# Optimization experiments

Hardware: AMD Instinct MI355X
Metric: run time of the kernel (lower is better)

## Reference

```python
import jax, jax.numpy as jnp
import numpy as np

G = 64        # grid_size
S = 4         # num_samples along perpendicular axis
C = 771       # feature_channels
NH = 3        # n_heads
NV = 4        # number of camera views
HF = WF = 64  # image feature map size
B = 1
QD = 3 * C    # query_dim of TriplaneAttention


def bilin(img, gx, gy, padding):
    """Bilinear grid_sample, align_corners=True. img [C,H,W]; gx,gy normalized [-1,1]."""
    Ci, H, W = img.shape
    ix = (gx + 1.0) * 0.5 * (W - 1)
    iy = (gy + 1.0) * 0.5 * (H - 1)
    if padding == 'border':
        ix = jnp.clip(ix, 0, W - 1)
        iy = jnp.clip(iy, 0, H - 1)
    x0 = jnp.floor(ix); y0 = jnp.floor(iy)
    x1 = x0 + 1.0;      y1 = y0 + 1.0
    wx = ix - x0;       wy = iy - y0
    img2 = img.reshape(Ci, H * W)
    def gather(xi, yi):
        xc = jnp.clip(xi, 0, W - 1).astype(jnp.int32)
        yc = jnp.clip(yi, 0, H - 1).astype(jnp.int32)
        vals = jnp.take(img2, (yc * W + xc).reshape(-1), axis=1).reshape((Ci,) + xi.shape)
        if padding == 'zeros':
            valid = ((xi >= 0) & (xi <= W - 1) & (yi >= 0) & (yi <= H - 1)).astype(img.dtype)
            vals = vals * valid
        return vals
    return (gather(x0, y0) * ((1 - wx) * (1 - wy)) + gather(x1, y0) * (wx * (1 - wy))
            + gather(x0, y1) * ((1 - wx) * wy) + gather(x1, y1) * (wx * wy))


def sample_points_along_axis(plane):
    x = jnp.linspace(-1.0, 1.0, G)
    gx, gy = jnp.meshgrid(x, x, indexing='xy')  # [G,G]
    samp = jnp.linspace(-1.0, 1.0, S)
    ex = jnp.broadcast_to(gx[..., None], (G, G, S))
    ey = jnp.broadcast_to(gy[..., None], (G, G, S))
    es = jnp.broadcast_to(samp[None, None, :], (G, G, S))
    if plane == 'xy':
        return jnp.stack([ex, ey, es], axis=-1)
    elif plane == 'xz':
        return jnp.stack([ex, es, ey], axis=-1)
    else:
        return jnp.stack([es, ex, ey], axis=-1)


def project_to_other_planes(points, plane, queries):
    # points [G,G,S,3]; queries = [q_xy, q_xz, q_yz] each [G,G,C]
    idx = {'xy': 0, 'xz': 1, 'yz': 2}
    sel = {'xy': (0, 1), 'xz': (0, 2), 'yz': (1, 2)}
    feats = []
    for other in ['xy', 'xz', 'yz']:
        if other == plane:
            continue
        a, b = sel[other]
        coords = jnp.stack([points[..., a], points[..., b]], axis=-1)
        # Faithful to original: pixel-range coords passed as normalized grid, border padding
        g = jnp.clip((coords * 0.5 + 0.5) * (G - 1), 0, G - 1)
        pf = queries[idx[other]].transpose(2, 0, 1)  # [C,G,G]
        s = bilin(pf, g[..., 0], g[..., 1], 'border')  # [C,G,G,S]
        feats.append(s.transpose(1, 2, 3, 0))          # [G,G,S,C]
    return jnp.concatenate(feats, axis=2)              # [G,G,2S,C]


def layernorm(x, g, b):
    mu = jnp.mean(x, axis=-1, keepdims=True)
    var = jnp.mean((x - mu) ** 2, axis=-1, keepdims=True)
    return (x - mu) / jnp.sqrt(var + 1e-5) * g + b


def triplane_attention(query, context, Wk, bk, Wv, bv, ln_g, ln_b):
    # query [B,N,QD]; context [B,N,L,C]
    Bq, N, L, _ = context.shape
    DH = QD // NH
    q = layernorm(query, ln_g, ln_b).reshape(Bq, N, NH, DH)
    k = (context @ Wk + bk).reshape(Bq, N, L, NH, DH)
    v = (context @ Wv + bv).reshape(Bq, N, L, NH, DH)
    scores = jnp.einsum('bnlhd,bnhd->bhnl', k, q)   # no 1/sqrt(d) scaling (faithful)
    w = jax.nn.softmax(scores, axis=-1)
    out = jnp.einsum('bhnl,bnlhd->bnhd', w, v)
    return out.reshape(Bq, N, QD)


def setup_inputs():
    key = jax.random.key(0)
    ks = jax.random.split(key, 12)
    image_features = jax.random.normal(ks[0], (B, NV, C, HF, WF), jnp.float32)
    depths = jax.random.uniform(ks[1], (B, NV, HF, WF), jnp.float32)
    # cameras: identity rotation, w2c translation [dx,0,3] -> c2w translation [-dx,0,-3]
    offs = np.linspace(-0.2, 0.2, NV).astype(np.float32)
    c2w = np.tile(np.eye(4, dtype=np.float32), (B, NV, 1, 1))
    for m in range(NV):
        c2w[:, m, 0, 3] = -offs[m]
        c2w[:, m, 2, 3] = -3.0
    K = np.zeros((B, NV, 3, 3), np.float32)
    K[:, :, 0, 0] = WF; K[:, :, 1, 1] = HF
    K[:, :, 0, 2] = WF / 2; K[:, :, 1, 2] = HF / 2; K[:, :, 2, 2] = 1.0
    pointclouds = jax.random.uniform(ks[2], (B, 4096, 3), jnp.float32, minval=-1.0, maxval=1.0)
    q_xy = jax.random.normal(ks[3], (G, G, C), jnp.float32) * 0.02
    q_xz = jax.random.normal(ks[4], (G, G, C), jnp.float32) * 0.02
    q_yz = jax.random.normal(ks[5], (G, G, C), jnp.float32) * 0.02
    Wk = jax.random.normal(ks[6], (C, QD), jnp.float32) * 0.02
    bk = jnp.zeros((QD,), jnp.float32)
    Wv = jax.random.normal(ks[7], (C, QD), jnp.float32) * 0.02
    bv = jnp.zeros((QD,), jnp.float32)
    ln_g = jnp.ones((QD,), jnp.float32)
    ln_b = jnp.zeros((QD,), jnp.float32)
    return dict(image_features=image_features, depths=depths, c2w_cond=jnp.asarray(c2w),
                intrinsic_cond=jnp.asarray(K), pointclouds=pointclouds,
                q_xy=q_xy, q_xz=q_xz, q_yz=q_yz, Wk=Wk, bk=bk, Wv=Wv, bv=bv,
                ln_g=ln_g, ln_b=ln_b)


def _forward(image_features, c2w_cond, intrinsic_cond, q_xy, q_xz, q_yz,
             Wk, bk, Wv, bv, ln_g, ln_b):
    queries = [q_xy, q_xz, q_yz]
    w2c = jnp.linalg.inv(c2w_cond)  # [B,NV,4,4]

    def project(pts, w2c_b, K_b):
        # pts [N,3]; returns u,v,mask each [N,NV]
        ph = jnp.concatenate([pts, jnp.ones_like(pts[:, :1])], axis=-1)
        cam = jnp.einsum('nl,mkl->nmk', ph, w2c_b)      # [N,NV,4]
        depth = cam[..., 2]
        uvh = jnp.einsum('nmk,mhk->nmh', cam[..., :3], K_b)
        ds = depth + 1e-8
        u = uvh[..., 0] / ds
        v = uvh[..., 1] / ds
        mask = (depth > 0) & (u >= 0) & (u < WF) & (v >= 0) & (v < HF)
        return u, v, mask

    def sample_views(feats_b, u_b, v_b, mask_b):
        # feats_b [NV,C,HF,WF]; u_b,v_b [N,NV] -> [N,NV,C]
        gx = 2.0 * (u_b / (WF - 1)) - 1.0
        gy = 2.0 * (v_b / (HF - 1)) - 1.0
        samp = jax.vmap(lambda img, x, y: bilin(img, x, y, 'zeros'))(feats_b, gx.T, gy.T)  # [NV,C,N]
        samp = samp.transpose(2, 0, 1)  # [N,NV,C]
        return samp * mask_b[..., None].astype(samp.dtype)

    outs = []
    for pi, plane in enumerate(['xy', 'xz', 'yz']):
        points = sample_points_along_axis(plane)           # [G,G,S,3]
        pts = points.reshape(-1, 3)                        # [G*G*S,3]
        u, v, mask = jax.vmap(lambda w, k: project(pts, w, k))(w2c, intrinsic_cond)  # [B,N,NV]
        samp = jax.vmap(sample_views)(image_features, u, v, mask)  # [B,N,NV,C]
        ctx = samp.reshape(B, G * G, S * NV, C)
        other = project_to_other_planes(points, plane, queries)    # [G,G,2S,C]
        q = jnp.concatenate([queries[pi],
                             jnp.mean(other[:, :, :S], axis=2),
                             jnp.mean(other[:, :, S:], axis=2)], axis=-1).reshape(G * G, QD)
        q = jnp.broadcast_to(q[None], (B, G * G, QD))
        out = triplane_attention(q, ctx, Wk, bk, Wv, bv, ln_g, ln_b)
        outs.append(out.reshape(B, G, G, QD))
    return tuple(outs)


def reference(image_features, depths, c2w_cond, intrinsic_cond, pointclouds,
              q_xy, q_xz, q_yz, Wk, bk, Wv, bv, ln_g, ln_b):
    return _forward(image_features, c2w_cond, intrinsic_cond,
                    q_xy, q_xz, q_yz, Wk, bk, Wv, bv, ln_g, ln_b)
```

## Files before the change

### kernel.cpp

```cpp
#include <hip/hip_runtime.h>
#include <math.h>


constexpr int kG = 64, kS = 4, kC = 771, kNV = 4;
constexpr int kQD = 2313;
constexpr int kNPIX = 4096;
constexpr int kL = 16;
constexpr int kImgMStride = kC * kG * kG;
constexpr int kKP = 800;
constexpr int kLDA = 2400;
constexpr int kBROWS = 896;
constexpr int kCP = 776;
constexpr int kNG = kCP / 4;
constexpr int kLDQ = 3 * kCP;
constexpr int kIMS2 = kNPIX * kCP;

constexpr size_t kQKB_FLOATS = (size_t)kNPIX * kLDQ;
constexpr size_t kW_ELEMS = (size_t)3 * kBROWS * kKP;
constexpr size_t kA0_ELEMS = (size_t)kNPIX * kKP;
constexpr size_t kWH_ELEMS = (size_t)kNPIX * kLDA;
constexpr size_t kQN_FLOATS = (size_t)kNPIX * kQD;
constexpr size_t kTAB_FLOATS = (size_t)6 * 64 * kC;

using bf16x8 = __attribute__((ext_vector_type(8))) short;
// ... 387 lines not shown
        for (int r = 0; r < 4; ++r) {
          const int row = rbase + i * 16 + (lane >> 4) * 4 + r;
          const float mu = mr[2 * row], rs = mr[2 * row + 1];
          dst[(size_t)row * kLDQ + col] = rs * acc[i][j][r] - rs * mu * uu + vv;
        }
      } else if (col < kCP) {
#pragma unroll
        for (int r = 0; r < 4; ++r) {
          const int row = rbase + i * 16 + (lane >> 4) * 4 + r;
          dst[(size_t)row * kLDQ + col] = 0.f;
        }
      }
    }
  }
}

__global__ void __launch_bounds__(256) gemm_tab_kernel(
    const unsigned short* __restrict__ Thi,
    const unsigned short* __restrict__ Tlo,
    const unsigned short* __restrict__ Wkhi,
    const unsigned short* __restrict__ Wklo, float* __restrict__ Atab) {
  __shared__ unsigned short smA[2][128 * 32];
  __shared__ unsigned short smB[2][128 * 32];
  const int t = blockIdx.y;
  const int n0 = blockIdx.x * 128;
  const int h = 1 + (t & 1);
  const unsigned short* Ah = Thi + (size_t)t * 128 * kKP;
  const unsigned short* Al = Tlo + (size_t)t * 128 * kKP;
  const unsigned short* Bh = Wkhi + (size_t)h * kBROWS * kKP;
  const unsigned short* Bl = Wklo + (size_t)h * kBROWS * kKP;
  const int tid = threadIdx.x;
  const int lane = tid & 63, w = tid >> 6;
  const int wm = w >> 1, wn = w & 1;

  const int sr0 = w * 16 + (lane >> 2);
  const int ss = lane & 3;
  size_t aoff[2], boff[2];
  int ldsb[2];
#pragma unroll
  for (int p = 0; p < 2; ++p) {
    const int r = p * 64 + sr0;
    const int kl = (ss ^ ((r >> 1) & 3)) * 8;
    aoff[p] = (size_t)r * kKP + kl;
    boff[p] = (size_t)(n0 + r) * kKP + kl;
    ldsb[p] = (p * 64 + w * 16) * 32;
  }
  int offA[4], offB[4];
#pragma unroll
  for (int i = 0; i < 4; ++i) {
    const int ra = wm * 64 + i * 16 + (lane & 15);
    offA[i] = ra * 32 + (((lane >> 4) ^ ((ra >> 1) & 3)) << 3);
    const int rb = wn * 64 + i * 16 + (lane & 15);
    offB[i] = rb * 32 + (((lane >> 4) ^ ((rb >> 1) & 3)) << 3);
  }
  f32x4 acc[4][4];
#pragma unroll
  for (int i = 0; i < 4; ++i)
#pragma unroll
    for (int j = 0; j < 4; ++j) acc[i][j] = f32x4{0.f, 0.f, 0.f, 0.f};

  for (int k0 = 0; k0 < kKP; k0 += 32) {
#pragma unroll
    for (int p = 0; p < 2; ++p) {
      gload16(Ah + aoff[p] + k0, &smA[0][ldsb[p]]);
      gload16(Al + aoff[p] + k0, &smA[1][ldsb[p]]);
      gload16(Bh + boff[p] + k0, &smB[0][ldsb[p]]);
      gload16(Bl + boff[p] + k0, &smB[1][ldsb[p]]);
    }
    __syncthreads();
    bf16x8 ah[4], al[4], bh[4], bl[4];
#pragma unroll
    for (int i = 0; i < 4; ++i) {
      ah[i] = *(const bf16x8*)&smA[0][offA[i]];
      al[i] = *(const bf16x8*)&smA[1][offA[i]];
      bh[i] = *(const bf16x8*)&smB[0][offB[i]];
      bl[i] = *(const bf16x8*)&smB[1][offB[i]];
    }
#pragma unroll
    for (int i = 0; i < 4; ++i)
#pragma unroll
      for (int j = 0; j < 4; ++j)
        acc[i][j] = __builtin_amdgcn_mfma_f32_16x16x32_bf16(ah[i], bh[j],
                                                            acc[i][j], 0, 0, 0);
#pragma unroll
    for (int i = 0; i < 4; ++i)
#pragma unroll
      for (int j = 0; j < 4; ++j)
        acc[i][j] = __builtin_amdgcn_mfma_f32_16x16x32_bf16(ah[i], bl[j],
                                                            acc[i][j], 0, 0, 0);
#pragma unroll
    for (int i = 0; i < 4; ++i)
#pragma unroll
      for (int j = 0; j < 4; ++j)
        acc[i][j] = __builtin_amdgcn_mfma_f32_16x16x32_bf16(al[i], bh[j],
                                                            acc[i][j], 0, 0, 0);
    __syncthreads();
  }

  float* C = Atab + (size_t)t * 128 * kCP;
  const int rbase = wm * 64;
  const int cbase = n0 + wn * 64;
#pragma unroll
  for (int i = 0; i < 4; ++i) {
#pragma unroll
    for (int j = 0; j < 4; ++j) {
      const int col = cbase + j * 16 + (lane & 15);
      if (col < kCP) {
        const float keep = (col < kC) ? 1.f : 0.f;
#pragma unroll
        for (int r = 0; r < 4; ++r) {
          const int row = rbase + i * 16 + (lane >> 4) * 4 + r;
          C[(size_t)row * kCP + col] = acc[i][j][r] * keep;
        }
      }
    }
  }
}

__global__ void __launch_bounds__(256) combine_qk_kernel(
    const float* __restrict__ Atab, const float* __restrict__ u,
    const float* __restrict__ v, const float* __restrict__ murs,
    float* __restrict__ qkb) {
  const int slot = blockIdx.y, n = blockIdx.x;
  const int i = n >> 6, j = n & 63, tid = threadIdx.x;
  const float mu = murs[2 * ((size_t)slot * kNPIX + n)];
  const float rs = murs[2 * ((size_t)slot * kNPIX + n) + 1];
  const float rsmu = rs * mu;
  float* dst = qkb + (size_t)slot * kQKB_FLOATS + (size_t)n * kLDQ;
  const float* A1 = Atab + ((size_t)(slot * 2 + 0) * 128 + j) * kCP;
  const float* A2 = Atab + ((size_t)(slot * 2 + 1) * 128 + i) * kCP;
  if (tid < kNG) {
    const int c4 = tid << 2;
    const float4 a1 = *(const float4*)&A1[c4];
    const float4 u1 = *(const float4*)&u[kCP + c4];
    const float4 v1 = *(const float4*)&v[kCP + c4];
    float4 r1;
    r1.x = rs * a1.x - rsmu * u1.x + v1.x;
    r1.y = rs * a1.y - rsmu * u1.y + v1.y;
    r1.z = rs * a1.z - rsmu * u1.z + v1.z;
    r1.w = rs * a1.w - rsmu * u1.w + v1.w;
    *(float4*)&dst[kCP + c4] = r1;
    const float4 a2 = *(const float4*)&A2[c4];
    const float4 u2 = *(const float4*)&u[2 * kCP + c4];
    const float4 v2 = *(const float4*)&v[2 * kCP + c4];
    float4 r2;
    r2.x = rs * a2.x - rsmu * u2.x + v2.x;
    r2.y = rs * a2.y - rsmu * u2.y + v2.y;
    r2.z = rs * a2.z - rsmu * u2.z + v2.z;
    r2.w = rs * a2.w - rsmu * u2.w + v2.w;
    *(float4*)&dst[2 * kCP + c4] = r2;
  }
}

__global__ void __launch_bounds__(512, 6) sample_attn4_kernel(
    const float* __restrict__ imgt, const float* __restrict__ w2c,
    const float* __restrict__ Kin, const float* __restrict__ qkb,
    const float* __restrict__ qbk, unsigned short* __restrict__ whi) {
  __shared__ __align__(16) float ctx[kL][kCP];
  __shared__ float sW2[kL][4];
  __shared__ int sI2[kL][4];
  __shared__ float sscp[2][48];
  __shared__ float ssc[48], swt[48];
  const int slot = blockIdx.y, plane = slot;
  const int bid = blockIdx.x;
  const int xcd = bid & 7, tt = bid >> 3;
  const int i = (xcd << 3) | ((tt >> 3) & 7);
  const int j = (((tt >> 6) << 3) | (tt & 7));
  const int n = (i << 6) | j;
  const int tid = threadIdx.x;
  const float* qkn = qkb + (size_t)slot * kQKB_FLOATS + (size_t)n * kLDQ;

  if (tid < kL) {
    const int s = tid >> 2, m = tid & 3;
    const float Xi = -1.f + 2.f * i / 63.f;
    const float Xj = -1.f + 2.f * j / 63.f;
    const float Ts = -1.f + 2.f * s / 3.f;
    float px, py, pz;
    if (plane == 0) { px = Xj; py = Xi; pz = Ts; }
    else if (plane == 1) { px = Xj; py = Ts; pz = Xi; }
    else { px = Ts; py = Xj; pz = Xi; }
    const float* W = w2c + m * 16;
    const float c0 = W[0] * px + W[1] * py + W[2] * pz + W[3];
    const float c1 = W[4] * px + W[5] * py + W[6] * pz + W[7];
    const float c2 = W[8] * px + W[9] * py + W[10] * pz + W[11];
    const float* Km = Kin + m * 9;
    const float un = Km[0] * c0 + Km[1] * c1 + Km[2] * c2;
    const float vn = Km[3] * c0 + Km[4] * c1 + Km[5] * c2;
    const float ds = c2 + 1e-8f;
    const float u = un / ds, v = vn / ds;
    const bool mk =
        (c2 > 0.f && u >= 0.f && u < 64.f && v >= 0.f && v < 64.f);
    float w00 = 0.f, w10 = 0.f, w01 = 0.f, w11 = 0.f;
    int i00 = 0, i10 = 0, i01 = 0, i11 = 0;
    if (mk) {
      const float gx = 2.f * (u / 63.f) - 1.f;
      const float gy = 2.f * (v / 63.f) - 1.f;
      const float ix = (gx + 1.f) * 0.5f * 63.f;
      const float iy = (gy + 1.f) * 0.5f * 63.f;
      const float x0 = floorf(ix), y0 = floorf(iy);
      const float x1 = x0 + 1.f, y1 = y0 + 1.f;
      const float wx = ix - x0, wy = iy - y0;
      const float v00 = (x0 >= 0.f && x0 <= 63.f && y0 >= 0.f && y0 <= 63.f) ? 1.f : 0.f;
      const float v10 = (x1 >= 0.f && x1 <= 63.f && y0 >= 0.f && y0 <= 63.f) ? 1.f : 0.f;
      const float v01 = (x0 >= 0.f && x0 <= 63.f && y1 >= 0.f && y1 <= 63.f) ? 1.f : 0.f;
      const float v11 = (x1 >= 0.f && x1 <= 63.f && y1 >= 0.f && y1 <= 63.f) ? 1.f : 0.f;
      w00 = (1.f - wx) * (1.f - wy) * v00;
      w10 = wx * (1.f - wy) * v10;
      w01 = (1.f - wx) * wy * v01;
      w11 = wx * wy * v11;
      const int x0i = (int)fminf(fmaxf(x0, 0.f), 63.f);
      const int x1i = (int)fminf(fmaxf(x1, 0.f), 63.f);
      const int y0i = (int)fminf(fmaxf(y0, 0.f), 63.f);
      const int y1i = (int)fminf(fmaxf(y1, 0.f), 63.f);
      const int mb = m * kIMS2;
      i00 = mb + (y0i * 64 + x0i) * kCP;
      i10 = mb + (y0i * 64 + x1i) * kCP;
      i01 = mb + (y1i * 64 + x0i) * kCP;
      i11 = mb + (y1i * 64 + x1i) * kCP;
    }
    sI2[tid][0] = i00; sI2[tid][1] = i10; sI2[tid][2] = i01; sI2[tid][3] = i11;
    sW2[tid][0] = w00; sW2[tid][1] = w10; sW2[tid][2] = w01; sW2[tid][3] = w11;
  }
  __syncthreads();

  const int lane = tid & 63, wv = tid >> 6;
#pragma unroll
  for (int q = 0; q < 2; ++q) {
    const int l = (wv << 1) + q;
    const float a0 = sW2[l][0], a1 = sW2[l][1], a2 = sW2[l][2], a3 = sW2[l][3];
    const int b0 = sI2[l][0], b1 = sI2[l][1], b2 = sI2[l][2], b3 = sI2[l][3];
    for (int g = lane; g < kNG; g += 64) {
      const int c4 = g << 2;
      const float4 t0 = *(const float4*)&imgt[b0 + c4];
      const float4 t1 = *(const float4*)&imgt[b1 + c4];
      const float4 t2 = *(const float4*)&imgt[b2 + c4];
      const float4 t3 = *(const float4*)&imgt[b3 + c4];
      float4 r;
      r.x = fmaf(t0.x, a0, fmaf(t1.x, a1, fmaf(t2.x, a2, t3.x * a3)));
      r.y = fmaf(t0.y, a0, fmaf(t1.y, a1, fmaf(t2.y, a2, t3.y * a3)));
      r.z = fmaf(t0.z, a0, fmaf(t1.z, a1, fmaf(t2.z, a2, t3.z * a3)));
      r.w = fmaf(t0.w, a0, fmaf(t1.w, a1, fmaf(t2.w, a2, t3.w * a3)));
      *(float4*)&ctx[l][c4] = r;
    }
  }
  __syncthreads();

  const int g16 = tid >> 4, l16 = tid & 15;
  const float* qbkn = qbk + ((size_t)slot * kNPIX + n) * 3;
  {
    const int l = g16 & 15, half = g16 >> 4;
    float p0 = 0.f, p1 = 0.f, p2 = 0.f;
#pragma unroll
    for (int it = 0; it < 6; ++it) {
      const int c4 = (l16 + ((2 * it + half) << 4)) << 2;
      const float4 cv = *(const float4*)&ctx[l][c4];
      const float4 q0 = *(const float4*)&qkn[c4];
      const float4 q1 = *(const float4*)&qkn[kCP + c4];
      const float4 q2 = *(const float4*)&qkn[2 * kCP + c4];
      p0 = fmaf(cv.x, q0.x, fmaf(cv.y, q0.y, fmaf(cv.z, q0.z, fmaf(cv.w, q0.w, p0))));
      p1 = fmaf(cv.x, q1.x, fmaf(cv.y, q1.y, fmaf(cv.z, q1.z, fmaf(cv.w, q1.w, p1))));
      p2 = fmaf(cv.x, q2.x, fmaf(cv.y, q2.y, fmaf(cv.z, q2.z, fmaf(cv.w, q2.w, p2))));
    }
    if (half == 0 && l16 < 2) {
      const int c4 = (192 + l16) << 2;
      const float4 cv = *(const float4*)&ctx[l][c4];
      const float4 q0 = *(const float4*)&qkn[c4];
      const float4 q1 = *(const float4*)&qkn[kCP + c4];
      const float4 q2 = *(const float4*)&qkn[2 * kCP + c4];
      p0 = fmaf(cv.x, q0.x, fmaf(cv.y, q0.y, fmaf(cv.z, q0.z, fmaf(cv.w, q0.w, p0))));
      p1 = fmaf(cv.x, q1.x, fmaf(cv.y, q1.y, fmaf(cv.z, q1.z, fmaf(cv.w, q1.w, p1))));
      p2 = fmaf(cv.x, q2.x, fmaf(cv.y, q2.y, fmaf(cv.z, q2.z, fmaf(cv.w, q2.w, p2))));
    }
#pragma unroll
    for (int off = 8; off; off >>= 1) {
      p0 += __shfl_down(p0, off, 16);
      p1 += __shfl_down(p1, off, 16);
      p2 += __shfl_down(p2, off, 16);
    }
    if (l16 == 0) {
      sscp[half][l] = p0;
      sscp[half][16 + l] = p1;
      sscp[half][32 + l] = p2;
    }
  }
  __syncthreads();
  if (tid < 48) ssc[tid] = sscp[0][tid] + sscp[1][tid] + qbkn[tid >> 4];
  __syncthreads();
  if (tid < 3) {
    float mx = ssc[tid * 16];
#pragma unroll
    for (int l = 1; l < kL; ++l) mx = fmaxf(mx, ssc[tid * 16 + l]);
    float e[kL];
    float sum = 0.f;
#pragma unroll
    for (int l = 0; l < kL; ++l) {
      e[l] = expf(ssc[tid * 16 + l] - mx);
      sum += e[l];
    }
    const float inv = 1.f / sum;
#pragma unroll
    for (int l = 0; l < kL; ++l) swt[tid * 16 + l] = e[l] * inv;
  }
  __syncthreads();

  unsigned short* wh = whi + (size_t)slot * kWH_ELEMS + (size_t)n * kLDA;
  if (tid < 2 * kNG) {
    const int c4 = (tid >> 1) << 2;
    const int l0 = (tid & 1) << 3;
    float4 o0{0.f, 0.f, 0.f, 0.f}, o1{0.f, 0.f, 0.f, 0.f},
        o2{0.f, 0.f, 0.f, 0.f};
#pragma unroll
    for (int dl = 0; dl < 8; ++dl) {
      const int l = l0 + dl;
      const float4 cv = *(const float4*)&ctx[l][c4];
      const float s0 = swt[l], s1 = swt[16 + l], s2 = swt[32 + l];
      o0.x = fmaf(cv.x, s0, o0.x); o0.y = fmaf(cv.y, s0, o0.y);
      o0.z = fmaf(cv.z, s0, o0.z); o0.w = fmaf(cv.w, s0, o0.w);
      o1.x = fmaf(cv.x, s1, o1.x); o1.y = fmaf(cv.y, s1, o1.y);
      o1.z = fmaf(cv.z, s1, o1.z); o1.w = fmaf(cv.w, s1, o1.w);
      o2.x = fmaf(cv.x, s2, o2.x); o2.y = fmaf(cv.y, s2, o2.y);
      o2.z = fmaf(cv.z, s2, o2.z); o2.w = fmaf(cv.w, s2, o2.w);
    }
    o0.x += __shfl_xor(o0.x, 1); o0.y += __shfl_xor(o0.y, 1);
    o0.z += __shfl_xor(o0.z, 1); o0.w += __shfl_xor(o0.w, 1);
    o1.x += __shfl_xor(o1.x, 1); o1.y += __shfl_xor(o1.y, 1);
    o1.z += __shfl_xor(o1.z, 1); o1.w += __shfl_xor(o1.w, 1);
    o2.x += __shfl_xor(o2.x, 1); o2.y += __shfl_xor(o2.y, 1);
    o2.z += __shfl_xor(o2.z, 1); o2.w += __shfl_xor(o2.w, 1);
    if ((tid & 1) == 0) {
      float4 ov[3] = {o0, o1, o2};
#pragma unroll
      for (int h = 0; h < 3; ++h) {
        ushort4 hi;
        hi.x = f2bf(ov[h].x);
        hi.y = f2bf(ov[h].y);
        hi.z = f2bf(ov[h].z);
        hi.w = f2bf(ov[h].w);
        *(ushort4*)&wh[h * kKP + c4] = hi;
      }
    }
  }
  if (tid < 72) {
    const int h = tid / 24, k2 = kCP + tid % 24;
    wh[h * kKP + k2] = 0;
  }
}

__global__ void __launch_bounds__(256) gemm_out_kernel(
    const unsigned short* __restrict__ Ahi,
    const unsigned short* __restrict__ Bhi, float* __restrict__ C,
    const float* __restrict__ bias) {
  __shared__ unsigned short smA[128 * 32];
  __shared__ unsigned short smB[128 * 32];
  const int slot = blockIdx.z / 3, h = blockIdx.z % 3;
  const int t = blockIdx.y * 7 + blockIdx.x;
  const int xcd = t & 7, idx = t >> 3;
  const int nb = idx % 7, mb = (xcd << 2) + idx / 7;
  const int m0 = mb * 128, n0 = nb * 128;
  const unsigned short* Ah = Ahi + (size_t)slot * kWH_ELEMS;
  float* Cs = C + (size_t)slot * kQN_FLOATS;
  const int tid = threadIdx.x;
  const int lane = tid & 63, w = tid >> 6;
  const int wm = w >> 1, wn = w & 1;

  const int sr0 = w * 16 + (lane >> 2);
  const int ss = lane & 3;
  size_t aoff[2], boff[2];
  int ldsb[2];
#pragma unroll
  for (int p = 0; p < 2; ++p) {
    const int r = p * 64 + sr0;
    const int kl = (ss ^ ((r >> 1) & 3)) * 8;
    aoff[p] = (size_t)(m0 + r) * kLDA + (size_t)h * kKP + kl;
    boff[p] = ((size_t)h * kBROWS + (n0 + r)) * kKP + kl;
    ldsb[p] = (p * 64 + w * 16) * 32;
  }
  int offA[4], offB[4];
#pragma unroll
  for (int i = 0; i < 4; ++i) {
    const int ra = wm * 64 + i * 16 + (lane & 15);
    offA[i] = ra * 32 + (((lane >> 4) ^ ((ra >> 1) & 3)) << 3);
    const int rb = wn * 64 + i * 16 + (lane & 15);
    offB[i] = rb * 32 + (((lane >> 4) ^ ((rb >> 1) & 3)) << 3);
  }
  f32x4 acc[4][4];
#pragma unroll
  for (int i = 0; i < 4; ++i)
#pragma unroll
    for (int j = 0; j < 4; ++j) acc[i][j] = f32x4{0.f, 0.f, 0.f, 0.f};

  for (int k0 = 0; k0 < kKP; k0 += 32) {
#pragma unroll
    for (int p = 0; p < 2; ++p) {
      gload16(Ah + aoff[p] + k0, &smA[ldsb[p]]);
      gload16(Bhi + boff[p] + k0, &smB[ldsb[p]]);
    }
    __syncthreads();
    bf16x8 ah[4], bh[4];
#pragma unroll
    for (int i = 0; i < 4; ++i) {
      ah[i] = *(const bf16x8*)&smA[offA[i]];
      bh[i] = *(const bf16x8*)&smB[offB[i]];
    }
#pragma unroll
    for (int i = 0; i < 4; ++i)
#pragma unroll
      for (int j = 0; j < 4; ++j)
        acc[i][j] = __builtin_amdgcn_mfma_f32_16x16x32_bf16(ah[i], bh[j],
                                                            acc[i][j], 0, 0, 0);
    __syncthreads();
  }

  const int rbase = m0 + wm * 64;
  const int cbase = n0 + wn * 64;
#pragma unroll
  for (int i = 0; i < 4; ++i) {
#pragma unroll
    for (int j = 0; j < 4; ++j) {
      const int col = cbase + j * 16 + (lane & 15);
      if (col < kC) {
        const float bb = bias[h * kC + col];
#pragma unroll
        for (int r = 0; r < 4; ++r) {
          const int row = rbase + i * 16 + (lane >> 4) * 4 + r;
          Cs[(size_t)row * kQD + h * kC + col] = acc[i][j][r] + bb;
        }
      }
    }
  }
}

__global__ void __launch_bounds__(256) build_q_f32(
    const float* __restrict__ q_xy, const float* __restrict__ q_xz,
    const float* __restrict__ q_yz, const int plane,
    const float* __restrict__ ln_g, const float* __restrict__ ln_b,
    const float* __restrict__ bk, float* __restrict__ qn,
    float* __restrict__ qbk) {
  const float* qp = (plane == 0) ? q_xy : (plane == 1) ? q_xz : q_yz;
  const float* qo0 = (plane == 0) ? q_xz : q_xy;
  const float* qo1 = (plane == 2) ? q_xz : q_yz;
  const int n = blockIdx.x, i = n >> 6, j = n & 63, tid = threadIdx.x;
  __shared__ float qf[kQD];
  __shared__ int sIdx[2][4][4];
  __shared__ float sW[2][4][4];
  __shared__ float red[16];

  if (tid < 8) {
    const int part = tid >> 2, s = tid & 3;
    const float Xi = -1.f + 2.f * i / 63.f;
    const float Xj = -1.f + 2.f * j / 63.f;
    const float Ts = -1.f + 2.f * s / 3.f;
    float a, b;
    if (plane == 0) { a = part ? Xi : Xj; b = Ts; }
    else if (plane == 1) {
      if (part == 0) { a = Xj; b = Ts; } else { a = Ts; b = Xi; }
    } else { a = Ts; b = part ? Xi : Xj; }
    const float ga = fminf(fmaxf((a * 0.5f + 0.5f) * 63.f, 0.f), 63.f);
    const float gb = fminf(fmaxf((b * 0.5f + 0.5f) * 63.f, 0.f), 63.f);
    const float ix = fminf(fmaxf((ga + 1.f) * 0.5f * 63.f, 0.f), 63.f);
    const float iy = fminf(fmaxf((gb + 1.f) * 0.5f * 63.f, 0.f), 63.f);
    const float x0 = floorf(ix), y0 = floorf(iy);
    const float wx = ix - x0, wy = iy - y0;
    const int x0i = (int)x0, y0i = (int)y0;
    const int x1i = (x0i + 1 > 63) ? 63 : x0i + 1;
    const int y1i = (y0i + 1 > 63) ? 63 : y0i + 1;
    sIdx[part][s][0] = (y0i * 64 + x0i) * kC;
    sIdx[part][s][1] = (y0i * 64 + x1i) * kC;
    sIdx[part][s][2] = (y1i * 64 + x0i) * kC;
    sIdx[part][s][3] = (y1i * 64 + x1i) * kC;
    sW[part][s][0] = (1.f - wx) * (1.f - wy);
    sW[part][s][1] = wx * (1.f - wy);
    sW[part][s][2] = (1.f - wx) * wy;
    sW[part][s][3] = wx * wy;
  }
  __syncthreads();
  for (int c = tid; c < kC; c += 256) {
    qf[c] = qp[(size_t)n * kC + c];
    float a1 = 0.f, a2 = 0.f;
#pragma unroll
    for (int s = 0; s < 4; ++s) {
      a1 += qo0[sIdx[0][s][0] + c] * sW[0][s][0]
          + qo0[sIdx[0][s][1] + c] * sW[0][s][1]
          + qo0[sIdx[0][s][2] + c] * sW[0][s][2]
          + qo0[sIdx[0][s][3] + c] * sW[0][s][3];
      a2 += qo1[sIdx[1][s][0] + c] * sW[1][s][0]
          + qo1[sIdx[1][s][1] + c] * sW[1][s][1]
          + qo1[sIdx[1][s][2] + c] * sW[1][s][2]
          + qo1[sIdx[1][s][3] + c] * sW[1][s][3];
    }
    qf[kC + c] = a1 * 0.25f;
    qf[2 * kC + c] = a2 * 0.25f;
// ... 191 lines not shown
  __shared__ float Bs[BK][BN + 4];
  const int hoff = blockIdx.z * hstride;
  const int m0 = blockIdx.y * BM, n0 = blockIdx.x * BN;
  const int tid = threadIdx.x;
  const int ty = tid >> 4, tx = tid & 15;
  float acc[8][4];
#pragma unroll
  for (int r = 0; r < 8; ++r)
#pragma unroll
    for (int c = 0; c < 4; ++c) acc[r][c] = 0.f;
  for (int k0 = 0; k0 < K; k0 += BK) {
#pragma unroll
    for (int p = 0; p < 8; ++p) {
      const int idx = tid + p * 256;
      const int mm = idx >> 4, kk = idx & 15;
      float v = 0.f;
      if (k0 + kk < K) v = A[(size_t)(m0 + mm) * lda + hoff + k0 + kk];
      As[kk][mm] = v;
    }
    if (BT) {
#pragma unroll
      for (int p = 0; p < 4; ++p) {
        const int idx = tid + p * 256;
        const int jj = idx >> 4, kk = idx & 15;
        float v = 0.f;
        if ((n0 + jj) < N && (k0 + kk) < K)
          v = B[(size_t)(n0 + jj) * ldb + hoff + k0 + kk];
        Bs[kk][jj] = v;
      }
    } else {
#pragma unroll
      for (int p = 0; p < 4; ++p) {
        const int idx = tid + p * 256;
        const int kk = idx >> 6, jj = idx & 63;
        float v = 0.f;
        if ((n0 + jj) < N && (k0 + kk) < K)
          v = B[(size_t)(k0 + kk) * ldb + hoff + n0 + jj];
        Bs[kk][jj] = v;
      }
    }
    __syncthreads();
#pragma unroll
    for (int kk = 0; kk < BK; ++kk) {
      float a[8], b[4];
#pragma unroll
      for (int r = 0; r < 8; ++r) a[r] = As[kk][ty * 8 + r];
#pragma unroll
      for (int c = 0; c < 4; ++c) b[c] = Bs[kk][tx * 4 + c];
#pragma unroll
      for (int r = 0; r < 8; ++r)
#pragma unroll
        for (int c = 0; c < 4; ++c) acc[r][c] = fmaf(a[r], b[c], acc[r][c]);
    }
    __syncthreads();
  }
#pragma unroll
  for (int r = 0; r < 8; ++r) {
    const int mm = m0 + ty * 8 + r;
    if (mm >= M) continue;
#pragma unroll
    for (int c = 0; c < 4; ++c) {
      const int jj = n0 + tx * 4 + c;
      if (jj < N) {
        float v = acc[r][c];
        if (BIAS) v += bias[hoff + jj];
        Cp[(size_t)mm * ldc + hoff + jj] = v;
      }
    }
  }
}

extern "C" void kernel_launch(void* const* d_in, const int* in_sizes, int n_in,
                              void* d_out, int out_size, void* d_ws,
                              size_t ws_size, hipStream_t stream) {
  const float* imgf = (const float*)d_in[0];
  const float* c2w = (const float*)d_in[2];
  const float* Kin = (const float*)d_in[3];
  const float* qpl[3] = {(const float*)d_in[5], (const float*)d_in[6],
                         (const float*)d_in[7]};
  const float* Wk = (const float*)d_in[8];
  const float* bk = (const float*)d_in[9];
  const float* Wv = (const float*)d_in[10];
  const float* bv = (const float*)d_in[11];
  const float* ln_g = (const float*)d_in[12];
  const float* ln_b = (const float*)d_in[13];
  float* out = (float*)d_out;
  char* wsb = (char*)d_ws;

  const size_t IMGT_FLOATS = (size_t)kNV * kIMS2;

  size_t off = 0;
  auto take = [&](size_t bytes) {
    size_t p = off;
    off = (off + bytes + 511) & ~(size_t)511;
    return p;
  };
  const size_t o_w2c = take(64 * 4);
  const size_t o_qbk = take((size_t)3 * kNPIX * 3 * 4);
  const size_t o_qkb = take((size_t)3 * kQKB_FLOATS * 4);
  const size_t o_wkhi = take(kW_ELEMS * 2);
  const size_t o_wklo = take(kW_ELEMS * 2);
  const size_t o_wvthi = take(kW_ELEMS * 2);
  const size_t o_a0hi = take((size_t)3 * kA0_ELEMS * 2);
  const size_t o_a0lo = take((size_t)3 * kA0_ELEMS * 2);
  const size_t o_whi = take((size_t)3 * kWH_ELEMS * 2);
  const size_t o_murs = take((size_t)3 * kNPIX * 2 * 4);
  const size_t o_u = take((size_t)3 * kCP * 4);
  const size_t o_v = take((size_t)3 * kCP * 4);
  const size_t o_tab = take(kTAB_FLOATS * 4);
  const size_t o_tshi = take((size_t)6 * 128 * kKP * 2);
  const size_t o_tslo = take((size_t)6 * 128 * kKP * 2);
  const size_t o_atab = take((size_t)6 * 128 * kCP * 4);
  const size_t o_imgt = take(IMGT_FLOATS * 4);
  const size_t need = off;

  if (ws_size >= need) {
    float* w2c = (float*)(wsb + o_w2c);
    float* qbk = (float*)(wsb + o_qbk);
    float* qkb = (float*)(wsb + o_qkb);
    unsigned short* wkhi = (unsigned short*)(wsb + o_wkhi);
    unsigned short* wklo = (unsigned short*)(wsb + o_wklo);
    unsigned short* wvthi = (unsigned short*)(wsb + o_wvthi);
    unsigned short* a0hi = (unsigned short*)(wsb + o_a0hi);
    unsigned short* a0lo = (unsigned short*)(wsb + o_a0lo);
    unsigned short* whi = (unsigned short*)(wsb + o_whi);
    float* murs = (float*)(wsb + o_murs);
    float* uvec = (float*)(wsb + o_u);
    float* vvec = (float*)(wsb + o_v);
    float* meantab = (float*)(wsb + o_tab);
    unsigned short* tshi = (unsigned short*)(wsb + o_tshi);
    unsigned short* tslo = (unsigned short*)(wsb + o_tslo);
    float* atab = (float*)(wsb + o_atab);
    float* imgt = (float*)(wsb + o_imgt);

    invert4_kernel<<<1, 64, 0, stream>>>(c2w, w2c);
    prep_wk_kernel<<<dim3(kBROWS, 3), 256, 0, stream>>>(Wk, wkhi, wklo);
    prep_wvt_kernel<<<dim3(13, 14, 3), 256, 0, stream>>>(Wv, wvthi);
    prep_meantab_kernel<<<dim3(64, 6), 256, 0, stream>>>(qpl[0], qpl[1],
                                                         qpl[2], meantab);
    prep_tabsplit_kernel<<<dim3(128, 6), 256, 0, stream>>>(meantab, ln_g,
                                                           tshi, tslo);
    prep_uv_kernel<<<dim3(kCP, 3), 256, 0, stream>>>(Wk, ln_g, ln_b, uvec,
                                                     vvec);
    transpose_img_kernel<<<dim3(64, kNV), 256, 0, stream>>>(imgf, imgt);
    gemm_tab_kernel<<<dim3(7, 6), 256, 0, stream>>>(tshi, tslo, wkhi, wklo,
                                                    atab);
    build_a0_kernel<<<dim3(kNPIX, 3), 256, 0, stream>>>(
        qpl[0], qpl[1], qpl[2], meantab, ln_g, ln_b, bk, a0hi, a0lo, murs,
        qbk);
    gemm_a0_kernel<<<dim3(7, 32, 3), 256, 0, stream>>>(
        a0hi, a0lo, wkhi, wklo, murs, uvec, vvec, qkb);
    combine_qk_kernel<<<dim3(kNPIX, 3), 256, 0, stream>>>(atab, uvec, vvec,
                                                          murs, qkb);
    sample_attn4_kernel<<<dim3(kNPIX, 3), 512, 0, stream>>>(
        imgt, w2c, Kin, qkb, qbk, whi);
    gemm_out_kernel<<<dim3(7, 32, 9), 256, 0, stream>>>(whi, wvthi, out, bv);
  } else {
    float* ws = (float*)d_ws;
    const size_t OFF_QBK = 64;
    const size_t OFF_BIG = OFF_QBK + (size_t)kNPIX * 3;
    float* w2c = ws;
    float* qbk = ws + OFF_QBK;
    float* qn = ws + OFF_BIG;
    float* qkb = qn + kQN_FLOATS;

    invert4_kernel<<<1, 64, 0, stream>>>(c2w, w2c);
    for (int p = 0; p < 3; ++p) {
      build_q_f32<<<kNPIX, 256, 0, stream>>>(qpl[0], qpl[1], qpl[2], p, ln_g,
                                             ln_b, bk, qn, qbk);
      gemm_f32<true, false><<<dim3(13, 32, 3), 256, 0, stream>>>(
          qn, Wk, qkb, nullptr, kNPIX, kC, kC, kQD, kQD, kQD, kC);
      sample_attn_f32<<<kNPIX, 256, 0, stream>>>(imgf, w2c, Kin, qkb, qbk, p,
                                                 qn);
      gemm_f32<false, true><<<dim3(13, 32, 3), 256, 0, stream>>>(
          qn, Wv, out + (size_t)p * kQN_FLOATS, bv, kNPIX, kC, kC, kQD, kQD,
          kQD, kC);
    }
  }
}
```

Measured before the change: 585.7 us.

## Process sampling-attention context in two chunks with online softmax to halve LDS

The fused sample+attention kernel now builds the 16-entry context in two chunks of 8 rows instead of holding all 16 rows in shared memory. Softmax becomes an online (running max/sum with rescale) update, and normalisation is deferred to the final write. This roughly halves shared memory per block, allowing launch bounds to rise from 6 to 8 blocks per CU for more latency hiding. In exchange it adds extra barriers, the rescale arithmetic, and more qk global loads (qkn is reread once per chunk).

```diff
diff --git a/kernel.cpp b/kernel.cpp
--- a/kernel.cpp
+++ b/kernel.cpp
@@ -563,15 +563,17 @@
   }
 }
 
-__global__ void __launch_bounds__(512, 6) sample_attn4_kernel(
+__global__ void __launch_bounds__(512, 8) sample_attn6_kernel(
     const float* __restrict__ imgt, const float* __restrict__ w2c,
     const float* __restrict__ Kin, const float* __restrict__ qkb,
     const float* __restrict__ qbk, unsigned short* __restrict__ whi) {
-  __shared__ __align__(16) float ctx[kL][kCP];
+  __shared__ __align__(16) float ctx8[8][kCP];
   __shared__ float sW2[kL][4];
   __shared__ int sI2[kL][4];
-  __shared__ float sscp[2][48];
-  __shared__ float ssc[48], swt[48];
+  __shared__ float sscp[4][24];
+  __shared__ float ssc[24];
+  __shared__ float swts[3][8];
+  __shared__ float smax[3], ssum[3], srf[3];
   const int slot = blockIdx.y, plane = slot;
   const int bid = blockIdx.x;
   const int xcd = bid & 7, tt = bid >> 3;
@@ -632,106 +634,128 @@
     sI2[tid][0] = i00; sI2[tid][1] = i10; sI2[tid][2] = i01; sI2[tid][3] = i11;
     sW2[tid][0] = w00; sW2[tid][1] = w10; sW2[tid][2] = w01; sW2[tid][3] = w11;
   }
+  if (tid < 3) {
+    smax[tid] = -INFINITY;
+    ssum[tid] = 0.f;
+  }
   __syncthreads();
 
   const int lane = tid & 63, wv = tid >> 6;
-#pragma unroll
-  for (int q = 0; q < 2; ++q) {
-    const int l = (wv << 1) + q;
-    const float a0 = sW2[l][0], a1 = sW2[l][1], a2 = sW2[l][2], a3 = sW2[l][3];
-    const int b0 = sI2[l][0], b1 = sI2[l][1], b2 = sI2[l][2], b3 = sI2[l][3];
-    for (int g = lane; g < kNG; g += 64) {
-      const int c4 = g << 2;
-      const float4 t0 = *(const float4*)&imgt[b0 + c4];
-      const float4 t1 = *(const float4*)&imgt[b1 + c4];
-      const float4 t2 = *(const float4*)&imgt[b2 + c4];
-      const float4 t3 = *(const float4*)&imgt[b3 + c4];
-      float4 r;
-      r.x = fmaf(t0.x, a0, fmaf(t1.x, a1, fmaf(t2.x, a2, t3.x * a3)));
-      r.y = fmaf(t0.y, a0, fmaf(t1.y, a1, fmaf(t2.y, a2, t3.y * a3)));
-      r.z = fmaf(t0.z, a0, fmaf(t1.z, a1, fmaf(t2.z, a2, t3.z * a3)));
-      r.w = fmaf(t0.w, a0, fmaf(t1.w, a1, fmaf(t2.w, a2, t3.w * a3)));
-      *(float4*)&ctx[l][c4] = r;
-    }
-  }
-  __syncthreads();
-
-  const int g16 = tid >> 4, l16 = tid & 15;
   const float* qbkn = qbk + ((size_t)slot * kNPIX + n) * 3;
-  {
-    const int l = g16 & 15, half = g16 >> 4;
-    float p0 = 0.f, p1 = 0.f, p2 = 0.f;
-#pragma unroll
-    for (int it = 0; it < 6; ++it) {
-      const int c4 = (l16 + ((2 * it + half) << 4)) << 2;
-      const float4 cv = *(const float4*)&ctx[l][c4];
-      const float4 q0 = *(const float4*)&qkn[c4];
-      const float4 q1 = *(const float4*)&qkn[kCP + c4];
-      const float4 q2 = *(const float4*)&qkn[2 * kCP + c4];
-      p0 = fmaf(cv.x, q0.x, fmaf(cv.y, q0.y, fmaf(cv.z, q0.z, fmaf(cv.w, q0.w, p0))));
-      p1 = fmaf(cv.x, q1.x, fmaf(cv.y, q1.y, fmaf(cv.z, q1.z, fmaf(cv.w, q1.w, p1))));
-      p2 = fmaf(cv.x, q2.x, fmaf(cv.y, q2.y, fmaf(cv.z, q2.z, fmaf(cv.w, q2.w, p2))));
-    }
-    if (half == 0 && l16 < 2) {
-      const int c4 = (192 + l16) << 2;
-      const float4 cv = *(const float4*)&ctx[l][c4];
-      const float4 q0 = *(const float4*)&qkn[c4];
-      const float4 q1 = *(const float4*)&qkn[kCP + c4];
-      const float4 q2 = *(const float4*)&qkn[2 * kCP + c4];
-      p0 = fmaf(cv.x, q0.x, fmaf(cv.y, q0.y, fmaf(cv.z, q0.z, fmaf(cv.w, q0.w, p0))));
-      p1 = fmaf(cv.x, q1.x, fmaf(cv.y, q1.y, fmaf(cv.z, q1.z, fmaf(cv.w, q1.w, p1))));
-      p2 = fmaf(cv.x, q2.x, fmaf(cv.y, q2.y, fmaf(cv.z, q2.z, fmaf(cv.w, q2.w, p2))));
-    }
-#pragma unroll
-    for (int off = 8; off; off >>= 1) {
-      p0 += __shfl_down(p0, off, 16);
-      p1 += __shfl_down(p1, off, 16);
-      p2 += __shfl_down(p2, off, 16);
-    }
-    if (l16 == 0) {
-      sscp[half][l] = p0;
-      sscp[half][16 + l] = p1;
-      sscp[half][32 + l] = p2;
-    }
-  }
-  __syncthreads();
-  if (tid < 48) ssc[tid] = sscp[0][tid] + sscp[1][tid] + qbkn[tid >> 4];
-  __syncthreads();
-  if (tid < 3) {
-    float mx = ssc[tid * 16];
-#pragma unroll
-    for (int l = 1; l < kL; ++l) mx = fmaxf(mx, ssc[tid * 16 + l]);
-    float e[kL];
-    float sum = 0.f;
-#pragma unroll
-    for (int l = 0; l < kL; ++l) {
-      e[l] = expf(ssc[tid * 16 + l] - mx);
-      sum += e[l];
-    }
-    const float inv = 1.f / sum;
-#pragma unroll
-    for (int l = 0; l < kL; ++l) swt[tid * 16 + l] = e[l] * inv;
-  }
-  __syncthreads();
+  float4 o0{0.f, 0.f, 0.f, 0.f}, o1{0.f, 0.f, 0.f, 0.f},
+      o2{0.f, 0.f, 0.f, 0.f};
+  const int pvc4 = (tid >> 1) << 2;
+  const int pvhalf = tid & 1;
+
+  for (int chunk = 0; chunk < 2; ++chunk) {
+    {
+      const int l = (chunk << 3) + wv;
+      const float a0 = sW2[l][0], a1 = sW2[l][1], a2 = sW2[l][2],
+                  a3 = sW2[l][3];
+      const int b0 = sI2[l][0], b1 = sI2[l][1], b2 = sI2[l][2],
+                b3 = sI2[l][3];
+      for (int g = lane; g < kNG; g += 64) {
+        const int c4 = g << 2;
+        const float4 t0 = *(const float4*)&imgt[b0 + c4];
+        const float4 t1 = *(const float4*)&imgt[b1 + c4];
+        const float4 t2 = *(const float4*)&imgt[b2 + c4];
+        const float4 t3 = *(const float4*)&imgt[b3 + c4];
+        float4 r;
+        r.x = fmaf(t0.x, a0, fmaf(t1.x, a1, fmaf(t2.x, a2, t3.x * a3)));
+        r.y = fmaf(t0.y, a0, fmaf(t1.y, a1, fmaf(t2.y, a2, t3.y * a3)));
+        r.z = fmaf(t0.z, a0, fmaf(t1.z, a1, fmaf(t2.z, a2, t3.z * a3)));
+        r.w = fmaf(t0.w, a0, fmaf(t1.w, a1, fmaf(t2.w, a2, t3.w * a3)));
+        *(float4*)&ctx8[wv][c4] = r;
+      }
+    }
+    __syncthreads();
+
+    {
+      const int g16 = tid >> 4, l16 = tid & 15;
+      const int lq = g16 & 7, quarter = g16 >> 3;
+      float p0 = 0.f, p1 = 0.f, p2 = 0.f;
+#pragma unroll
+      for (int it = 0; it < 3; ++it) {
+        const int c4 = (l16 + ((4 * it + quarter) << 4)) << 2;
+        const float4 cv = *(const float4*)&ctx8[lq][c4];
+        const float4 q0 = *(const float4*)&qkn[c4];
+        const float4 q1 = *(const float4*)&qkn[kCP + c4];
+        const float4 q2 = *(const float4*)&qkn[2 * kCP + c4];
+        p0 = fmaf(cv.x, q0.x, fmaf(cv.y, q0.y, fmaf(cv.z, q0.z, fmaf(cv.w, q0.w, p0))));
+        p1 = fmaf(cv.x, q1.x, fmaf(cv.y, q1.y, fmaf(cv.z, q1.z, fmaf(cv.w, q1.w, p1))));
+        p2 = fmaf(cv.x, q2.x, fmaf(cv.y, q2.y, fmaf(cv.z, q2.z, fmaf(cv.w, q2.w, p2))));
+      }
+      if (quarter == 0 && l16 < 2) {
+        const int c4 = (192 + l16) << 2;
+        const float4 cv = *(const float4*)&ctx8[lq][c4];
+        const float4 q0 = *(const float4*)&qkn[c4];
+        const float4 q1 = *(const float4*)&qkn[kCP + c4];
+        const float4 q2 = *(const float4*)&qkn[2 * kCP + c4];
+        p0 = fmaf(cv.x, q0.x, fmaf(cv.y, q0.y, fmaf(cv.z, q0.z, fmaf(cv.w, q0.w, p0))));
+        p1 = fmaf(cv.x, q1.x, fmaf(cv.y, q1.y, fmaf(cv.z, q1.z, fmaf(cv.w, q1.w, p1))));
+        p2 = fmaf(cv.x, q2.x, fmaf(cv.y, q2.y, fmaf(cv.z, q2.z, fmaf(cv.w, q2.w, p2))));
+      }
+#pragma unroll
+      for (int off = 8; off; off >>= 1) {
+        p0 += __shfl_down(p0, off, 16);
+        p1 += __shfl_down(p1, off, 16);
+        p2 += __shfl_down(p2, off, 16);
+      }
+      if (l16 == 0) {
+        sscp[quarter][lq] = p0;
+        sscp[quarter][8 + lq] = p1;
+        sscp[quarter][16 + lq] = p2;
+      }
+    }
+    __syncthreads();
+    if (tid < 24)
+      ssc[tid] = sscp[0][tid] + sscp[1][tid] + sscp[2][tid] + sscp[3][tid] +
+                 qbkn[tid >> 3];
+    __syncthreads();
+    if (tid < 3) {
+      const int h = tid;
+      float cm = ssc[h * 8];
+#pragma unroll
+      for (int l = 1; l < 8; ++l) cm = fmaxf(cm, ssc[h * 8 + l]);
+      const float mold = smax[h];
+      const float mnew = fmaxf(mold, cm);
+      const float rf = expf(mold - mnew);
+      float s = 0.f;
+#pragma unroll
+      for (int l = 0; l < 8; ++l) {
+        const float e = expf(ssc[h * 8 + l] - mnew);
+        swts[h][l] = e;
+        s += e;
+      }
+      ssum[h] = ssum[h] * rf + s;
+      smax[h] = mnew;
+      srf[h] = rf;
+    }
+    __syncthreads();
+
+    if (tid < 2 * kNG) {
+      const float r0 = srf[0], r1 = srf[1], r2 = srf[2];
+      o0.x *= r0; o0.y *= r0; o0.z *= r0; o0.w *= r0;
+      o1.x *= r1; o1.y *= r1; o1.z *= r1; o1.w *= r1;
+      o2.x *= r2; o2.y *= r2; o2.z *= r2; o2.w *= r2;
+#pragma unroll
+      for (int dl = 0; dl < 4; ++dl) {
+        const int l = (pvhalf << 2) + dl;
+        const float4 cv = *(const float4*)&ctx8[l][pvc4];
+        const float s0 = swts[0][l], s1 = swts[1][l], s2 = swts[2][l];
+        o0.x = fmaf(cv.x, s0, o0.x); o0.y = fmaf(cv.y, s0, o0.y);
+        o0.z = fmaf(cv.z, s0, o0.z); o0.w = fmaf(cv.w, s0, o0.w);
+        o1.x = fmaf(cv.x, s1, o1.x); o1.y = fmaf(cv.y, s1, o1.y);
+        o1.z = fmaf(cv.z, s1, o1.z); o1.w = fmaf(cv.w, s1, o1.w);
+        o2.x = fmaf(cv.x, s2, o2.x); o2.y = fmaf(cv.y, s2, o2.y);
+        o2.z = fmaf(cv.z, s2, o2.z); o2.w = fmaf(cv.w, s2, o2.w);
+      }
+    }
+    __syncthreads();
+  }
 
   unsigned short* wh = whi + (size_t)slot * kWH_ELEMS + (size_t)n * kLDA;
   if (tid < 2 * kNG) {
-    const int c4 = (tid >> 1) << 2;
-    const int l0 = (tid & 1) << 3;
-    float4 o0{0.f, 0.f, 0.f, 0.f}, o1{0.f, 0.f, 0.f, 0.f},
-        o2{0.f, 0.f, 0.f, 0.f};
-#pragma unroll
-    for (int dl = 0; dl < 8; ++dl) {
-      const int l = l0 + dl;
-      const float4 cv = *(const float4*)&ctx[l][c4];
-      const float s0 = swt[l], s1 = swt[16 + l], s2 = swt[32 + l];
-      o0.x = fmaf(cv.x, s0, o0.x); o0.y = fmaf(cv.y, s0, o0.y);
-      o0.z = fmaf(cv.z, s0, o0.z); o0.w = fmaf(cv.w, s0, o0.w);
-      o1.x = fmaf(cv.x, s1, o1.x); o1.y = fmaf(cv.y, s1, o1.y);
-      o1.z = fmaf(cv.z, s1, o1.z); o1.w = fmaf(cv.w, s1, o1.w);
-      o2.x = fmaf(cv.x, s2, o2.x); o2.y = fmaf(cv.y, s2, o2.y);
-      o2.z = fmaf(cv.z, s2, o2.z); o2.w = fmaf(cv.w, s2, o2.w);
-    }
     o0.x += __shfl_xor(o0.x, 1); o0.y += __shfl_xor(o0.y, 1);
     o0.z += __shfl_xor(o0.z, 1); o0.w += __shfl_xor(o0.w, 1);
     o1.x += __shfl_xor(o1.x, 1); o1.y += __shfl_xor(o1.y, 1);
@@ -739,7 +763,15 @@
     o2.x += __shfl_xor(o2.x, 1); o2.y += __shfl_xor(o2.y, 1);
     o2.z += __shfl_xor(o2.z, 1); o2.w += __shfl_xor(o2.w, 1);
     if ((tid & 1) == 0) {
-      float4 ov[3] = {o0, o1, o2};
+      const float in0 = 1.f / ssum[0], in1 = 1.f / ssum[1],
+                  in2 = 1.f / ssum[2];
+      float4 ov[3];
+      ov[0].x = o0.x * in0; ov[0].y = o0.y * in0;
+      ov[0].z = o0.z * in0; ov[0].w = o0.w * in0;
+      ov[1].x = o1.x * in1; ov[1].y = o1.y * in1;
+      ov[1].z = o1.z * in1; ov[1].w = o1.w * in1;
+      ov[2].x = o2.x * in2; ov[2].y = o2.y * in2;
+      ov[2].z = o2.z * in2; ov[2].w = o2.w * in2;
 #pragma unroll
       for (int h = 0; h < 3; ++h) {
         ushort4 hi;
@@ -747,7 +779,7 @@
         hi.y = f2bf(ov[h].y);
         hi.z = f2bf(ov[h].z);
         hi.w = f2bf(ov[h].w);
-        *(ushort4*)&wh[h * kKP + c4] = hi;
+        *(ushort4*)&wh[h * kKP + pvc4] = hi;
       }
     }
   }
@@ -1245,7 +1277,7 @@
         a0hi, a0lo, wkhi, wklo, murs, uvec, vvec, qkb);
     combine_qk_kernel<<<dim3(kNPIX, 3), 256, 0, stream>>>(atab, uvec, vvec,
                                                           murs, qkb);
-    sample_attn4_kernel<<<dim3(kNPIX, 3), 512, 0, stream>>>(
+    sample_attn6_kernel<<<dim3(kNPIX, 3), 512, 0, stream>>>(
         imgt, w2c, Kin, qkb, qbk, whi);
     gemm_out_kernel<<<dim3(7, 32, 9), 256, 0, stream>>>(whi, wvthi, out, bv);
   } else {
```

Result: slower. 894.6 us (+52.7%).
